# Kernel optimization log

Measured on AMD Instinct MI355X. Metric: run time of the kernel, lower is better.

Reference implementation:

```python
import jax, jax.numpy as jnp
import numpy as np

N = 100000   # nodes
R = 3        # relations
E = 500000   # edges per relation
F_IN, F_HID, F_OUT = 256, 128, 64


def setup_inputs() -> dict:
    key = jax.random.key(0)
    ks = jax.random.split(key, 9)
    feature = jax.random.normal(ks[0], (N, F_IN), jnp.float32)
    src = jax.random.randint(ks[1], (R, E), 0, N)
    dst = jax.random.randint(ks[2], (R, E), 0, N)
    neg_src = jax.random.randint(ks[3], (E,), 0, N)
    neg_dst = jax.random.randint(ks[4], (E,), 0, N)
    W1 = jax.random.normal(ks[5], (R, F_IN, F_HID), jnp.float32) * 0.05
    b1 = jnp.zeros((R, F_HID), jnp.float32)
    W2 = jax.random.normal(ks[6], (R, F_HID, F_OUT), jnp.float32) * 0.05
    b2 = jnp.zeros((R, F_OUT), jnp.float32)
    return {"feature": feature, "W1": W1, "b1": b1, "W2": W2, "b2": b2,
            "src": src, "dst": dst, "neg_src": neg_src, "neg_dst": neg_dst}


def _graph_conv(h, src, dst, W, b):
    """DGL GraphConv with norm='both': D_dst^-1/2 A (D_src^-1/2 h W) + b."""
    ones = jnp.ones(src.shape[0], h.dtype)
    out_deg = jnp.clip(jax.ops.segment_sum(ones, src, num_segments=N), 1.0)
    in_deg = jnp.clip(jax.ops.segment_sum(ones, dst, num_segments=N), 1.0)
    # project before gather (in_feats >= out_feats, same trick as DGL)
    x = (h * (out_deg ** -0.5)[:, None]) @ W          # [N, Fout]
    agg = jax.ops.segment_sum(x[src], dst, num_segments=N)  # gather-scatter
    return agg * (in_deg ** -0.5)[:, None] + b


def _hetero_layer(h, src, dst, W, b):
    # HeteroGraphConv: per-relation conv, mean-aggregate across relations
    conv = jax.vmap(_graph_conv, in_axes=(None, 0, 0, 0, 0))
    return conv(h, src, dst, W, b).mean(axis=0)


def reference(feature, W1, b1, W2, b2, src, dst, neg_src, neg_dst):
    h = jax.nn.relu(_hetero_layer(feature, src, dst, W1, b1))
    h = _hetero_layer(h, src, dst, W2, b2)             # [N, F_OUT]
    # HeteroDotProductPredictor: u_dot_v on etype (relation 0) / neg graph
    pos_score = jnp.sum(h[src[0]] * h[dst[0]], axis=-1)
    neg_score = jnp.sum(h[neg_src] * h[neg_dst], axis=-1)
    return jnp.stack([pos_score, neg_score])           # [2, E]
```

## Files before the change

### kernel.cpp

```cpp
#include <hip/hip_runtime.h>

namespace {
constexpr int NN   = 100000;
constexpr int RR   = 3;
constexpr int EE   = 500000;
constexpr int FIN  = 256;
constexpr int FHID = 128;
constexpr int FOUT = 64;
constexpr int EEC  = RR * EE;
constexpr int SCAN_TILE = 4096;
constexpr int NB = (NN + SCAN_TILE - 1) / SCAN_TILE;
constexpr int NCHUNK  = 8;
constexpr int CH      = NN / NCHUNK;
constexpr int GH      = 50;
constexpr int SLICE   = EE / GH;
constexpr int NCHUNK_F = 16;
constexpr int CH_F     = NN / NCHUNK_F;
}

typedef float f32x4  __attribute__((ext_vector_type(4)));
typedef short bf16x8 __attribute__((ext_vector_type(8)));

__device__ inline unsigned bf16round(float a) {
    unsigned u = __float_as_uint(a);
    return (u + 0x7FFFu + ((u >> 16) & 1u)) >> 16;
}
__device__ inline unsigned pack2_bf16(float a, float b) {
    return bf16round(a) | (bf16round(b) << 16);
}
__device__ inline float bflo(unsigned u) { return __uint_as_float(u << 16); }
__device__ inline float bfhi(unsigned u) { return __uint_as_float(u & 0xFFFF0000u); }

__device__ inline void gload_lds16(const unsigned short* g, unsigned short* l) {
    __builtin_amdgcn_global_load_lds(
        (const __attribute__((address_space(1))) void*)g,
        (__attribute__((address_space(3))) void*)l, 16, 0, 0);
}

__global__ __launch_bounds__(256) void convw_kernel(
    const float* __restrict__ W1, unsigned short* __restrict__ Wt1,
    const float* __restrict__ W2, unsigned short* __restrict__ Wt2)
{
    int idx = blockIdx.x * 256 + threadIdx.x;
    const int n1 = RR * FIN * FHID;
    const int n2 = RR * FHID * FOUT;
    if (idx < n1) {
        int r = idx / (FIN * FHID);
        int rem = idx - r * FIN * FHID;
        int k = rem / FHID, m = rem - k * FHID;
        Wt1[((size_t)r * FHID + m) * FIN + k] = (unsigned short)bf16round(W1[idx]);
    } else if (idx - n1 < n2) {
        int j = idx - n1;
        int r = j / (FHID * FOUT);
        int rem = j - r * FHID * FOUT;
        int k = rem / FOUT, m = rem - k * FOUT;
        Wt2[((size_t)r * FOUT + m) * FHID + k] = (unsigned short)bf16round(W2[j]);
    }
}

__global__ __launch_bounds__(512) void hist_deg_kernel(
    const int* __restrict__ src, const int* __restrict__ dst,
    unsigned short* __restrict__ partial_in, unsigned short* __restrict__ partial_out)
{
    __shared__ int cnt[CH];
    const int b   = blockIdx.x;
    const int dir = b / (RR * NCHUNK * GH);
    const int rem = b % (RR * NCHUNK * GH);
    const int r   = rem / (NCHUNK * GH);
    const int c   = (rem / GH) % NCHUNK;
    const int g   = rem % GH;
    const int tid = threadIdx.x;

    for (int i = tid; i < CH; i += 512) cnt[i] = 0;
    __syncthreads();

    const int* ids = (dir ? src : dst) + (size_t)r * EE + (size_t)g * SLICE;
    const int base = c * CH;
    for (int i4 = tid; i4 < SLICE / 4; i4 += 512) {
        int4 q = reinterpret_cast<const int4*>(ids)[i4];
        int d;
        d = q.x - base; if ((unsigned)d < (unsigned)CH) atomicAdd(&cnt[d], 1);
        d = q.y - base; if ((unsigned)d < (unsigned)CH) atomicAdd(&cnt[d], 1);
        d = q.z - base; if ((unsigned)d < (unsigned)CH) atomicAdd(&cnt[d], 1);
        d = q.w - base; if ((unsigned)d < (unsigned)CH) atomicAdd(&cnt[d], 1);
    }
    __syncthreads();

    unsigned short* part = (dir ? partial_out : partial_in)
                           + (size_t)g * RR * NN + (size_t)r * NN + base;
    for (int i = tid; i < CH; i += 512) part[i] = (unsigned short)cnt[i];
}

__global__ __launch_bounds__(256) void reduce_deg_kernel(
    const unsigned short* __restrict__ partial_in,
    const unsigned short* __restrict__ partial_out,
    int* __restrict__ deg_in, float* __restrict__ s_in, float* __restrict__ s_out)
{
    int idx = blockIdx.x * 256 + threadIdx.x;
    if (idx >= 2 * RR * NN) return;
    int dir = idx / (RR * NN);
    int j   = idx % (RR * NN);
    const unsigned short* part = dir ? partial_out : partial_in;
    int s = 0;
    #pragma unroll
    for (int g = 0; g < GH; ++g) s += part[(size_t)g * RR * NN + j];
    float v = rsqrtf((float)max(s, 1));
    if (dir == 0) { deg_in[j] = s; s_in[j] = v; }
    else          { s_out[j] = v; }
}

__global__ __launch_bounds__(1024) void scan_reduce_kernel(
    const int* __restrict__ deg_in, int* __restrict__ bsum)
{
    const int b = blockIdx.x;
    const int t = threadIdx.x;
    int n0 = b * SCAN_TILE + t * 4;
    int s = 0;
    if (n0 + 3 < NN) {
        int4 a = *reinterpret_cast<const int4*>(&deg_in[n0]);
        int4 bq = *reinterpret_cast<const int4*>(&deg_in[NN + n0]);
        int4 cq = *reinterpret_cast<const int4*>(&deg_in[2 * NN + n0]);
        s = a.x + a.y + a.z + a.w + bq.x + bq.y + bq.z + bq.w + cq.x + cq.y + cq.z + cq.w;
    } else {
        for (int i = 0; i < 4; ++i)
            if (n0 + i < NN)
                s += deg_in[n0 + i] + deg_in[NN + n0 + i] + deg_in[2 * NN + n0 + i];
    }
    __shared__ int sh[1024];
    sh[t] = s;
    __syncthreads();
    for (int off = 512; off > 0; off >>= 1) {
        if (t < off) sh[t] += sh[t + off];
        __syncthreads();
    }
    if (t == 0) bsum[b] = sh[0];
}

__global__ void scan_spine_kernel(int* __restrict__ bsum)
{
    if (threadIdx.x != 0 || blockIdx.x != 0) return;
    int run = 0;
    for (int i = 0; i < NB; ++i) {
        int v = bsum[i];
        bsum[i] = run;
        run += v;
    }
}

__global__ __launch_bounds__(1024) void scan_final_kernel(
    const int* __restrict__ deg_in, const int* __restrict__ bsum,
    int* __restrict__ rp_c)
{
    const int b = blockIdx.x;
    const int t = threadIdx.x;
    int n0 = b * SCAN_TILE + t * 4;
    int v[4] = {0, 0, 0, 0};
    for (int i = 0; i < 4; ++i)
        if (n0 + i < NN)
            v[i] = deg_in[n0 + i] + deg_in[NN + n0 + i] + deg_in[2 * NN + n0 + i];
    int s = v[0] + v[1] + v[2] + v[3];
    __shared__ int sh[1024];
    sh[t] = s;
    __syncthreads();
    for (int off = 1; off < 1024; off <<= 1) {
        int x = (t >= off) ? sh[t - off] : 0;
        __syncthreads();
        if (t >= off) sh[t] += x;
        __syncthreads();
    }
    int off = bsum[b] + sh[t] - s;
    for (int i = 0; i < 4; ++i) {
        if (n0 + i < NN) { rp_c[n0 + i] = off; off += v[i]; }
    }
    if (b == NB - 1 && t == 0) rp_c[NN] = EEC;
}

__global__ __launch_bounds__(256) void slice_off_kernel(
    const int* __restrict__ rp_c, const unsigned short* __restrict__ partial_in,
    int* __restrict__ base_c)
{
    int n = blockIdx.x * 256 + threadIdx.x;
    if (n >= NN) return;
    int base = rp_c[n];
    #pragma unroll
    for (int g = 0; g < GH; ++g) {
        base_c[(size_t)g * NN + n] = base;
        const unsigned short* p = partial_in + (size_t)g * RR * NN + n;
        base += (int)p[0] + (int)p[NN] + (int)p[2 * NN];
    }
}

__global__ __launch_bounds__(1024) void fill3_kernel(
    const int* __restrict__ src, const int* __restrict__ dst,
    const int* __restrict__ base_c, const float* __restrict__ s_in,
    uint2* __restrict__ col2)
{
    __shared__ int cur[CH_F];
    const int b   = blockIdx.x;
    const int c   = b / GH;
    const int g   = b % GH;
    const int tid = threadIdx.x;
    const int base = c * CH_F;

    const int* so = base_c + (size_t)g * NN + base;
    for (int i = tid; i < CH_F; i += 1024) cur[i] = so[i];
    __syncthreads();

    for (int r = 0; r < RR; ++r) {
        const int* ds = dst + (size_t)r * EE + (size_t)g * SLICE;
        const int* ss = src + (size_t)r * EE + (size_t)g * SLICE;
        const float* si = s_in + (size_t)r * NN;
        const unsigned rbase = (unsigned)(r * NN);
        for (int i4 = tid; i4 < SLICE / 4; i4 += 1024) {
            int4 d4 = reinterpret_cast<const int4*>(ds)[i4];
            int4 s4 = reinterpret_cast<const int4*>(ss)[i4];
            int dl;
            dl = d4.x - base;
            if ((unsigned)dl < (unsigned)CH_F) {
                int pos = atomicAdd(&cur[dl], 1);
                col2[pos] = make_uint2(rbase + (unsigned)s4.x, __float_as_uint(si[d4.x]));
            }
            dl = d4.y - base;
            if ((unsigned)dl < (unsigned)CH_F) {
                int pos = atomicAdd(&cur[dl], 1);
                col2[pos] = make_uint2(rbase + (unsigned)s4.y, __float_as_uint(si[d4.y]));
            }
            dl = d4.z - base;
            if ((unsigned)dl < (unsigned)CH_F) {
                int pos = atomicAdd(&cur[dl], 1);
                col2[pos] = make_uint2(rbase + (unsigned)s4.z, __float_as_uint(si[d4.z]));
            }
            dl = d4.w - base;
            if ((unsigned)dl < (unsigned)CH_F) {
                int pos = atomicAdd(&cur[dl], 1);
                col2[pos] = make_uint2(rbase + (unsigned)s4.w, __float_as_uint(si[d4.w]));
            }
        }
    }
}

template<int K, int CN, bool A_F32>
__global__ __launch_bounds__(256) void gemm_v6_kernel(
    const void* __restrict__ Av, const unsigned short* __restrict__ Wt_base,
    const float* __restrict__ srow_base, unsigned short* __restrict__ C_base, int N)
{
    constexpr int BM  = 64;
    constexpr int BK  = 64;
    constexpr int MF  = 2;
    constexpr int NF  = 2;
    constexpr int LDA = A_F32 ? (BK + 8) : BK;

    __shared__ unsigned short As[BM * LDA];
    __shared__ unsigned short Bs[RR][64 * BK];
    __shared__ float sLds[RR][BM];

    const int tid  = threadIdx.x;
    const int wave = tid >> 6;
    const int lane = tid & 63;
    const int wr   = wave >> 1;
    const int wc   = wave & 1;
    const int row0 = blockIdx.x * BM;
    const int bh   = blockIdx.y;
    const int l15  = lane & 15;
    const int lq   = lane >> 4;

    for (int i = tid; i < RR * BM; i += 256) {
        int r  = i / BM;
        int rr = row0 + (i % BM);
        sLds[r][i % BM] = (rr < N) ? srow_base[(size_t)r * NN + rr] : 0.f;
    }

    f32x4 acc[RR][MF][NF];
    #pragma unroll
    for (int r = 0; r < RR; ++r)
        #pragma unroll
        for (int mi = 0; mi < MF; ++mi)
            #pragma unroll
            for (int ni = 0; ni < NF; ++ni)
                #pragma unroll
                for (int q = 0; q < 4; ++q) acc[r][mi][ni][q] = 0.0f;

    for (int k0 = 0; k0 < K; k0 += BK) {
        __syncthreads();
        if constexpr (A_F32) {
            const float* A = (const float*)Av;
            #pragma unroll
            for (int i = 0; i < 2; ++i) {
                int c2  = i * 256 + tid;
                int row = c2 >> 3;
                int fc  = (c2 & 7) * 2;
                float4 v0 = make_float4(0.f, 0.f, 0.f, 0.f);
                float4 v1 = make_float4(0.f, 0.f, 0.f, 0.f);
                if (row0 + row < N) {
                    const float* Ar = A + (size_t)(row0 + row) * K + k0 + fc * 4;
                    v0 = *reinterpret_cast<const float4*>(Ar);
                    v1 = *reinterpret_cast<const float4*>(Ar + 4);
                }
                uint4 o;
                o.x = pack2_bf16(v0.x, v0.y);
                o.y = pack2_bf16(v0.z, v0.w);
                o.z = pack2_bf16(v1.x, v1.y);
                o.w = pack2_bf16(v1.z, v1.w);
                *reinterpret_cast<uint4*>(&As[row * LDA + fc * 4]) = o;
            }
        } else {
            const unsigned short* A = (const unsigned short*)Av;
            #pragma unroll
            for (int i = 0; i < 2; ++i) {
                int c   = i * 256 + tid;
                int row = c >> 3;
                int kc  = c & 7;
                int kcs = kc ^ (row & 7);
                if (row0 + row < N)
                    gload_lds16(A + (size_t)(row0 + row) * K + k0 + kcs * 8, &As[c * 8]);
            }
        }
        #pragma unroll
        for (int i = 0; i < 6; ++i) {
            int c  = i * 256 + tid;
            int r  = c >> 9;
            int cc = c & 511;
            int n  = cc >> 3;
            int kc = cc & 7;
            int kcs = kc ^ (n & 7);
            gload_lds16(Wt_base + ((size_t)r * CN + bh * 64 + n) * K + k0 + kcs * 8,
                        &Bs[r][cc * 8]);
        }
        __syncthreads();

        #pragma unroll
        for (int kk = 0; kk < BK; kk += 32) {
            const int j = kk / 8 + lq;
            bf16x8 af[MF];
            #pragma unroll
            for (int mi = 0; mi < MF; ++mi) {
                int row = wr * 32 + mi * 16 + l15;
                if constexpr (A_F32)
                    af[mi] = *reinterpret_cast<const bf16x8*>(&As[row * LDA + kk + lq * 8]);
                else
                    af[mi] = *reinterpret_cast<const bf16x8*>(&As[row * BK + (j ^ (row & 7)) * 8]);
            }
            #pragma unroll
            for (int r = 0; r < RR; ++r) {
                bf16x8 bfg[NF];
                #pragma unroll
                for (int ni = 0; ni < NF; ++ni) {
                    int n = wc * 32 + ni * 16 + l15;
                    bfg[ni] = *reinterpret_cast<const bf16x8*>(&Bs[r][n * BK + (j ^ (n & 7)) * 8]);
                }
                #pragma unroll
                for (int mi = 0; mi < MF; ++mi)
                    #pragma unroll
                    for (int ni = 0; ni < NF; ++ni)
                        acc[r][mi][ni] = __builtin_amdgcn_mfma_f32_16x16x32_bf16(
                            af[mi], bfg[ni], acc[r][mi][ni], 0, 0, 0);
            }
        }
    }

    #pragma unroll
    for (int r = 0; r < RR; ++r) {
        unsigned short* C = C_base + (size_t)r * NN * CN;
        #pragma unroll
        for (int mi = 0; mi < MF; ++mi) {
            int lrow = wr * 32 + mi * 16 + lq * 4;
            #pragma unroll
            for (int ni = 0; ni < NF; ++ni) {
                int cc = bh * 64 + wc * 32 + ni * 16 + l15;
                #pragma unroll
                for (int q = 0; q < 4; ++q) {
                    int rr = row0 + lrow + q;
                    if (rr < N)
                        C[(size_t)rr * CN + cc] =
                            (unsigned short)bf16round(acc[r][mi][ni][q] * sLds[r][lrow + q]);
                }
            }
        }
    }
}

__global__ __launch_bounds__(256) void gather1_kernel(
    const unsigned* __restrict__ Y, const uint2* __restrict__ col2,
    const int* __restrict__ rp_c, const float* __restrict__ b1,
    unsigned* __restrict__ h1)
{
    const int wid  = threadIdx.x >> 6;
    const int lane = threadIdx.x & 63;
    const int n    = blockIdx.x * 4 + wid;
    if (n >= NN) return;
    const int beg = rp_c[n], end = rp_c[n + 1];

    float ax[8], ay[8];
    #pragma unroll
    for (int j = 0; j < 8; ++j) { ax[j] = 0.f; ay[j] = 0.f; }

    int e = beg;
    for (; e + 7 < end; e += 8) {
        uint2 cc[8]; unsigned uu[8];
        #pragma unroll
        for (int j = 0; j < 8; ++j) cc[j] = col2[e + j];
        #pragma unroll
        for (int j = 0; j < 8; ++j) uu[j] = Y[(size_t)cc[j].x * 64 + lane];
        #pragma unroll
        for (int j = 0; j < 8; ++j) {
            float s = __uint_as_float(cc[j].y);
            ax[j] = fmaf(s, bflo(uu[j]), ax[j]);
            ay[j] = fmaf(s, bfhi(uu[j]), ay[j]);
        }
    }
    for (; e + 3 < end; e += 4) {
        uint2 cc[4]; unsigned uu[4];
        #pragma unroll
        for (int j = 0; j < 4; ++j) cc[j] = col2[e + j];
        #pragma unroll
        for (int j = 0; j < 4; ++j) uu[j] = Y[(size_t)cc[j].x * 64 + lane];
        #pragma unroll
        for (int j = 0; j < 4; ++j) {
            float s = __uint_as_float(cc[j].y);
            ax[j] = fmaf(s, bflo(uu[j]), ax[j]);
            ay[j] = fmaf(s, bfhi(uu[j]), ay[j]);
        }
    }
    for (; e < end; ++e) {
        uint2 c0 = col2[e];
        unsigned u0 = Y[(size_t)c0.x * 64 + lane];
        float s = __uint_as_float(c0.y);
        ax[0] = fmaf(s, bflo(u0), ax[0]);
        ay[0] = fmaf(s, bfhi(u0), ay[0]);
    }
    float sx = ((ax[0] + ax[1]) + (ax[2] + ax[3])) + ((ax[4] + ax[5]) + (ax[6] + ax[7]));
    float sy = ((ay[0] + ay[1]) + (ay[2] + ay[3])) + ((ay[4] + ay[5]) + (ay[6] + ay[7]));
    float bx = b1[lane * 2]     + b1[FHID + lane * 2]     + b1[2 * FHID + lane * 2];
    float by = b1[lane * 2 + 1] + b1[FHID + lane * 2 + 1] + b1[2 * FHID + lane * 2 + 1];
    const float inv = 1.0f / (float)RR;
    float ox = fmaxf((sx + bx) * inv, 0.f);
    float oy = fmaxf((sy + by) * inv, 0.f);
    h1[(size_t)n * 64 + lane] = pack2_bf16(ox, oy);
}

__global__ __launch_bounds__(256) void gather2_kernel(
    const unsigned short* __restrict__ Y, const uint2* __restrict__ col2,
    const int* __restrict__ rp_c, const float* __restrict__ b2,
    unsigned short* __restrict__ h2)
{
    const int wid  = threadIdx.x >> 6;
    const int lane = threadIdx.x & 63;
    const int n    = blockIdx.x * 4 + wid;
    if (n >= NN) return;
    const int beg = rp_c[n], end = rp_c[n + 1];

    float a[8];
    #pragma unroll
    for (int j = 0; j < 8; ++j) a[j] = 0.f;

    int e = beg;
    for (; e + 7 < end; e += 8) {
        uint2 cc[8]; unsigned short uu[8];
        #pragma unroll
        for (int j = 0; j < 8; ++j) cc[j] = col2[e + j];
        #pragma unroll
        for (int j = 0; j < 8; ++j) uu[j] = Y[(size_t)cc[j].x * 64 + lane];
        #pragma unroll
        for (int j = 0; j < 8; ++j)
            a[j] = fmaf(__uint_as_float(cc[j].y),
                        __uint_as_float((unsigned)uu[j] << 16), a[j]);
    }
    for (; e + 3 < end; e += 4) {
        uint2 cc[4]; unsigned short uu[4];
        #pragma unroll
        for (int j = 0; j < 4; ++j) cc[j] = col2[e + j];
        #pragma unroll
        for (int j = 0; j < 4; ++j) uu[j] = Y[(size_t)cc[j].x * 64 + lane];
        #pragma unroll
        for (int j = 0; j < 4; ++j)
            a[j] = fmaf(__uint_as_float(cc[j].y),
                        __uint_as_float((unsigned)uu[j] << 16), a[j]);
    }
    for (; e < end; ++e) {
        uint2 c0 = col2[e];
        a[0] = fmaf(__uint_as_float(c0.y),
                    __uint_as_float((unsigned)Y[(size_t)c0.x * 64 + lane] << 16), a[0]);
    }
    float s = ((a[0] + a[1]) + (a[2] + a[3])) + ((a[4] + a[5]) + (a[6] + a[7]));
    float bs = b2[lane] + b2[FOUT + lane] + b2[2 * FOUT + lane];
    float o = (s + bs) * (1.0f / (float)RR);
    h2[(size_t)n * 64 + lane] = (unsigned short)bf16round(o);
}

__global__ __launch_bounds__(256) void score_kernel(
    const unsigned short* __restrict__ h, const int* __restrict__ src0,
    const int* __restrict__ dst0, const int* __restrict__ nsrc,
    const int* __restrict__ ndst, float* __restrict__ out)
{
    int idx = blockIdx.x * 256 + threadIdx.x;
    int e = idx >> 3;
    int l = idx & 7;
    int u, v;
    if (e < EE) { u = src0[e]; v = dst0[e]; }
    else        { u = nsrc[e - EE]; v = ndst[e - EE]; }
    uint4 a = *reinterpret_cast<const uint4*>(&h[(size_t)u * FOUT + l * 8]);
    uint4 b = *reinterpret_cast<const uint4*>(&h[(size_t)v * FOUT + l * 8]);
    float p = bflo(a.x) * bflo(b.x) + bfhi(a.x) * bfhi(b.x)
            + bflo(a.y) * bflo(b.y) + bfhi(a.y) * bfhi(b.y)
            + bflo(a.z) * bflo(b.z) + bfhi(a.z) * bfhi(b.z)
            + bflo(a.w) * bflo(b.w) + bfhi(a.w) * bfhi(b.w);
    p += __shfl_xor(p, 4, 8);
    p += __shfl_xor(p, 2, 8);
    p += __shfl_xor(p, 1, 8);
    if (l == 0) out[e] = p;
}

extern "C" void kernel_launch(void* const* d_in, const int* in_sizes, int n_in,
                              void* d_out, int out_size, void* d_ws, size_t ws_size,
                              hipStream_t stream)
{
    const float* feature = (const float*)d_in[0];
    const float* W1      = (const float*)d_in[1];
    const float* b1      = (const float*)d_in[2];
    const float* W2      = (const float*)d_in[3];
    const float* b2      = (const float*)d_in[4];
    const int*   src     = (const int*)d_in[5];
    const int*   dst     = (const int*)d_in[6];
    const int*   nsrc    = (const int*)d_in[7];
    const int*   ndst    = (const int*)d_in[8];
    float* out = (float*)d_out;

    char* p = (char*)d_ws;
    float* s_out   = (float*)p; p += sizeof(float) * RR * NN;
    float* s_in    = (float*)p; p += sizeof(float) * RR * NN;
    unsigned* h1   = (unsigned*)p; p += sizeof(unsigned) * (size_t)NN * 64;
    unsigned short* h2 = (unsigned short*)p; p += sizeof(unsigned short) * (size_t)NN * FOUT;
    char*  Yu      = p;         p += (size_t)RR * NN * FHID * 2;
    int*   deg_in  = (int*)p;   p += sizeof(int) * RR * NN;
    int*   rp_c    = (int*)p;   p += sizeof(int) * (NN + 1);
    uint2* col2    = (uint2*)p; p += sizeof(uint2) * (size_t)EEC;
    int*   bsum    = (int*)p;   p += sizeof(int) * NB;
    unsigned short* Wt1 = (unsigned short*)p; p += sizeof(unsigned short) * RR * FIN * FHID;
    unsigned short* Wt2 = (unsigned short*)p; p += sizeof(unsigned short) * RR * FHID * FOUT;

    unsigned short* Y1 = (unsigned short*)Yu;
    unsigned short* Y2 = (unsigned short*)Yu;
    unsigned short* partial_in  = (unsigned short*)Yu;
    unsigned short* partial_out = partial_in + (size_t)GH * RR * NN;
    int* base_c = (int*)partial_out;

    convw_kernel<<<(RR * FIN * FHID + RR * FHID * FOUT + 255) / 256, 256, 0, stream>>>(
        W1, Wt1, W2, Wt2);
    hist_deg_kernel<<<2 * RR * NCHUNK * GH, 512, 0, stream>>>(
        src, dst, partial_in, partial_out);
    reduce_deg_kernel<<<(2 * RR * NN + 255) / 256, 256, 0, stream>>>(
        partial_in, partial_out, deg_in, s_in, s_out);
    scan_reduce_kernel<<<NB, 1024, 0, stream>>>(deg_in, bsum);
    scan_spine_kernel<<<1, 64, 0, stream>>>(bsum);
    scan_final_kernel<<<NB, 1024, 0, stream>>>(deg_in, bsum, rp_c);
    slice_off_kernel<<<(NN + 255) / 256, 256, 0, stream>>>(rp_c, partial_in, base_c);
    fill3_kernel<<<NCHUNK_F * GH, 1024, 0, stream>>>(src, dst, base_c, s_in, col2);

    const int node_grid = (NN + 3) / 4;

    gemm_v6_kernel<FIN, FHID, true><<<dim3((NN + 63) / 64, 2), 256, 0, stream>>>(
        feature, Wt1, s_out, Y1, NN);
    gather1_kernel<<<node_grid, 256, 0, stream>>>(
        (const unsigned*)Y1, col2, rp_c, b1, h1);

    gemm_v6_kernel<FHID, FOUT, false><<<dim3((NN + 63) / 64, 1), 256, 0, stream>>>(
        h1, Wt2, s_out, Y2, NN);
    gather2_kernel<<<node_grid, 256, 0, stream>>>(
        Y2, col2, rp_c, b2, h2);

    score_kernel<<<(2 * EE * 8) / 256, 256, 0, stream>>>(h2, src, dst, nsrc, ndst, out);
}
```

Baseline: 341.6 us.

## Merge CSR fill kernel and layer-1 GEMM into one launch with block-range dispatch

Combines the edge fill into the CSR column array and the first-layer projection GEMM into a single kernel. The first FILL_BLOCKS block ids do the fill and the remaining ids do GEMM tiles, so the latency-bound, atomic-heavy fill can overlap with the MFMA GEMM instead of running serially. Fill blocks shrink from 1024 to 256 threads to match the GEMM block size, which means more loop iterations per block. Y1 shares memory with base_c, so GEMM writes can race with fill blocks still reading base_c if scheduling does not put the fill reads first.

```diff
diff --git a/kernel.cpp b/kernel.cpp
--- a/kernel.cpp
+++ b/kernel.cpp
@@ -16,6 +16,7 @@
 constexpr int SLICE   = EE / GH;
 constexpr int NCHUNK_F = 16;
 constexpr int CH_F     = NN / NCHUNK_F;
+constexpr int FILL_BLOCKS = NCHUNK_F * GH;
 }
 
 typedef float f32x4  __attribute__((ext_vector_type(4)));
@@ -190,50 +191,196 @@
     }
 }
 
-__global__ __launch_bounds__(1024) void fill3_kernel(
+template<int K, int CN, bool A_F32>
+__global__ __launch_bounds__(256) void mega_fill_gemm_kernel(
     const int* __restrict__ src, const int* __restrict__ dst,
     const int* __restrict__ base_c, const float* __restrict__ s_in,
-    uint2* __restrict__ col2)
-{
-    __shared__ int cur[CH_F];
-    const int b   = blockIdx.x;
-    const int c   = b / GH;
-    const int g   = b % GH;
+    uint2* __restrict__ col2,
+    const void* __restrict__ Av, const unsigned short* __restrict__ Wt_base,
+    const float* __restrict__ srow_base, unsigned short* __restrict__ C_base,
+    int N, int gemm_gx)
+{
+    constexpr int BM  = 64;
+    constexpr int BK  = 64;
+    constexpr int MF  = 2;
+    constexpr int NF  = 2;
+    constexpr int LDA = A_F32 ? (BK + 8) : BK;
+
+    __shared__ __align__(16) char smem[(size_t)BM * LDA * 2 + RR * 64 * BK * 2 + RR * BM * 4];
+
     const int tid = threadIdx.x;
-    const int base = c * CH_F;
-
-    const int* so = base_c + (size_t)g * NN + base;
-    for (int i = tid; i < CH_F; i += 1024) cur[i] = so[i];
-    __syncthreads();
-
+
+    if ((int)blockIdx.x < FILL_BLOCKS) {
+        int* cur = (int*)smem;
+        const int b    = blockIdx.x;
+        const int c    = b / GH;
+        const int g    = b % GH;
+        const int base = c * CH_F;
+
+        const int* so = base_c + (size_t)g * NN + base;
+        for (int i = tid; i < CH_F; i += 256) cur[i] = so[i];
+        __syncthreads();
+
+        for (int r = 0; r < RR; ++r) {
+            const int* ds = dst + (size_t)r * EE + (size_t)g * SLICE;
+            const int* ss = src + (size_t)r * EE + (size_t)g * SLICE;
+            const float* si = s_in + (size_t)r * NN;
+            const unsigned rbase = (unsigned)(r * NN);
+            for (int i4 = tid; i4 < SLICE / 4; i4 += 256) {
+                int4 d4 = reinterpret_cast<const int4*>(ds)[i4];
+                int4 s4 = reinterpret_cast<const int4*>(ss)[i4];
+                int dl;
+                dl = d4.x - base;
+                if ((unsigned)dl < (unsigned)CH_F) {
+                    int pos = atomicAdd(&cur[dl], 1);
+                    col2[pos] = make_uint2(rbase + (unsigned)s4.x, __float_as_uint(si[d4.x]));
+                }
+                dl = d4.y - base;
+                if ((unsigned)dl < (unsigned)CH_F) {
+                    int pos = atomicAdd(&cur[dl], 1);
+                    col2[pos] = make_uint2(rbase + (unsigned)s4.y, __float_as_uint(si[d4.y]));
+                }
+                dl = d4.z - base;
+                if ((unsigned)dl < (unsigned)CH_F) {
+                    int pos = atomicAdd(&cur[dl], 1);
+                    col2[pos] = make_uint2(rbase + (unsigned)s4.z, __float_as_uint(si[d4.z]));
+                }
+                dl = d4.w - base;
+                if ((unsigned)dl < (unsigned)CH_F) {
+                    int pos = atomicAdd(&cur[dl], 1);
+                    col2[pos] = make_uint2(rbase + (unsigned)s4.w, __float_as_uint(si[d4.w]));
+                }
+            }
+        }
+        return;
+    }
+
+    unsigned short* As  = (unsigned short*)smem;
+    unsigned short* Bs  = As + (size_t)BM * LDA;
+    float*          sLds = (float*)(Bs + (size_t)RR * 64 * BK);
+
+    const int gid  = (int)blockIdx.x - FILL_BLOCKS;
+    const int bx   = gid % gemm_gx;
+    const int bh   = gid / gemm_gx;
+    const int wave = tid >> 6;
+    const int lane = tid & 63;
+    const int wr   = wave >> 1;
+    const int wc   = wave & 1;
+    const int row0 = bx * BM;
+    const int l15  = lane & 15;
+    const int lq   = lane >> 4;
+
+    for (int i = tid; i < RR * BM; i += 256) {
+        int r  = i / BM;
+        int rr = row0 + (i % BM);
+        sLds[i] = (rr < N) ? srow_base[(size_t)r * NN + rr] : 0.f;
+    }
+
+    f32x4 acc[RR][MF][NF];
+    #pragma unroll
+    for (int r = 0; r < RR; ++r)
+        #pragma unroll
+        for (int mi = 0; mi < MF; ++mi)
+            #pragma unroll
+            for (int ni = 0; ni < NF; ++ni)
+                #pragma unroll
+                for (int q = 0; q < 4; ++q) acc[r][mi][ni][q] = 0.0f;
+
+    for (int k0 = 0; k0 < K; k0 += BK) {
+        __syncthreads();
+        if constexpr (A_F32) {
+            const float* A = (const float*)Av;
+            #pragma unroll
+            for (int i = 0; i < 2; ++i) {
+                int c2  = i * 256 + tid;
+                int row = c2 >> 3;
+                int fc  = (c2 & 7) * 2;
+                float4 v0 = make_float4(0.f, 0.f, 0.f, 0.f);
+                float4 v1 = make_float4(0.f, 0.f, 0.f, 0.f);
+                if (row0 + row < N) {
+                    const float* Ar = A + (size_t)(row0 + row) * K + k0 + fc * 4;
+                    v0 = *reinterpret_cast<const float4*>(Ar);
+                    v1 = *reinterpret_cast<const float4*>(Ar + 4);
+                }
+                uint4 o;
+                o.x = pack2_bf16(v0.x, v0.y);
+                o.y = pack2_bf16(v0.z, v0.w);
+                o.z = pack2_bf16(v1.x, v1.y);
+                o.w = pack2_bf16(v1.z, v1.w);
+                *reinterpret_cast<uint4*>(&As[row * LDA + fc * 4]) = o;
+            }
+        } else {
+            const unsigned short* A = (const unsigned short*)Av;
+            #pragma unroll
+            for (int i = 0; i < 2; ++i) {
+                int c   = i * 256 + tid;
+                int row = c >> 3;
+                int kc  = c & 7;
+                int kcs = kc ^ (row & 7);
+                if (row0 + row < N)
+                    gload_lds16(A + (size_t)(row0 + row) * K + k0 + kcs * 8, &As[c * 8]);
+            }
+        }
+        #pragma unroll
+        for (int i = 0; i < 6; ++i) {
+            int c  = i * 256 + tid;
+            int r  = c >> 9;
+            int cc = c & 511;
+            int n  = cc >> 3;
+            int kc = cc & 7;
+            int kcs = kc ^ (n & 7);
+            gload_lds16(Wt_base + ((size_t)r * CN + bh * 64 + n) * K + k0 + kcs * 8,
+                        &Bs[(size_t)r * 64 * BK + cc * 8]);
+        }
+        __syncthreads();
+
+        #pragma unroll
+        for (int kk = 0; kk < BK; kk += 32) {
+            const int j = kk / 8 + lq;
+            bf16x8 af[MF];
+            #pragma unroll
+            for (int mi = 0; mi < MF; ++mi) {
+                int row = wr * 32 + mi * 16 + l15;
+                if constexpr (A_F32)
+                    af[mi] = *reinterpret_cast<const bf16x8*>(&As[row * LDA + kk + lq * 8]);
+                else
+                    af[mi] = *reinterpret_cast<const bf16x8*>(&As[row * BK + (j ^ (row & 7)) * 8]);
+            }
+            #pragma unroll
+            for (int r = 0; r < RR; ++r) {
+                bf16x8 bfg[NF];
+                #pragma unroll
+                for (int ni = 0; ni < NF; ++ni) {
+                    int n = wc * 32 + ni * 16 + l15;
+                    bfg[ni] = *reinterpret_cast<const bf16x8*>(
+                        &Bs[(size_t)r * 64 * BK + n * BK + (j ^ (n & 7)) * 8]);
+                }
+                #pragma unroll
+                for (int mi = 0; mi < MF; ++mi)
+                    #pragma unroll
+                    for (int ni = 0; ni < NF; ++ni)
+                        acc[r][mi][ni] = __builtin_amdgcn_mfma_f32_16x16x32_bf16(
+                            af[mi], bfg[ni], acc[r][mi][ni], 0, 0, 0);
+            }
+        }
+    }
+
+    #pragma unroll
     for (int r = 0; r < RR; ++r) {
-        const int* ds = dst + (size_t)r * EE + (size_t)g * SLICE;
-        const int* ss = src + (size_t)r * EE + (size_t)g * SLICE;
-        const float* si = s_in + (size_t)r * NN;
-        const unsigned rbase = (unsigned)(r * NN);
-        for (int i4 = tid; i4 < SLICE / 4; i4 += 1024) {
-            int4 d4 = reinterpret_cast<const int4*>(ds)[i4];
-            int4 s4 = reinterpret_cast<const int4*>(ss)[i4];
-            int dl;
-            dl = d4.x - base;
-            if ((unsigned)dl < (unsigned)CH_F) {
-                int pos = atomicAdd(&cur[dl], 1);
-                col2[pos] = make_uint2(rbase + (unsigned)s4.x, __float_as_uint(si[d4.x]));
-            }
-            dl = d4.y - base;
-            if ((unsigned)dl < (unsigned)CH_F) {
-                int pos = atomicAdd(&cur[dl], 1);
-                col2[pos] = make_uint2(rbase + (unsigned)s4.y, __float_as_uint(si[d4.y]));
-            }
-            dl = d4.z - base;
-            if ((unsigned)dl < (unsigned)CH_F) {
-                int pos = atomicAdd(&cur[dl], 1);
-                col2[pos] = make_uint2(rbase + (unsigned)s4.z, __float_as_uint(si[d4.z]));
-            }
-            dl = d4.w - base;
-            if ((unsigned)dl < (unsigned)CH_F) {
-                int pos = atomicAdd(&cur[dl], 1);
-                col2[pos] = make_uint2(rbase + (unsigned)s4.w, __float_as_uint(si[d4.w]));
+        unsigned short* C = C_base + (size_t)r * NN * CN;
+        #pragma unroll
+        for (int mi = 0; mi < MF; ++mi) {
+            int lrow = wr * 32 + mi * 16 + lq * 4;
+            #pragma unroll
+            for (int ni = 0; ni < NF; ++ni) {
+                int cc = bh * 64 + wc * 32 + ni * 16 + l15;
+                #pragma unroll
+                for (int q = 0; q < 4; ++q) {
+                    int rr = row0 + lrow + q;
+                    if (rr < N)
+                        C[(size_t)rr * CN + cc] =
+                            (unsigned short)bf16round(acc[r][mi][ni][q] * sLds[r * BM + lrow + q]);
+                }
             }
         }
     }
@@ -554,16 +701,18 @@
     scan_spine_kernel<<<1, 64, 0, stream>>>(bsum);
     scan_final_kernel<<<NB, 1024, 0, stream>>>(deg_in, bsum, rp_c);
     slice_off_kernel<<<(NN + 255) / 256, 256, 0, stream>>>(rp_c, partial_in, base_c);
-    fill3_kernel<<<NCHUNK_F * GH, 1024, 0, stream>>>(src, dst, base_c, s_in, col2);
 
     const int node_grid = (NN + 3) / 4;
-
-    gemm_v6_kernel<FIN, FHID, true><<<dim3((NN + 63) / 64, 2), 256, 0, stream>>>(
-        feature, Wt1, s_out, Y1, NN);
+    const int gemm_gx = (NN + 63) / 64;
+
+    mega_fill_gemm_kernel<FIN, FHID, true><<<FILL_BLOCKS + gemm_gx * 2, 256, 0, stream>>>(
+        src, dst, base_c, s_in, col2,
+        feature, Wt1, s_out, Y1, NN, gemm_gx);
+
     gather1_kernel<<<node_grid, 256, 0, stream>>>(
         (const unsigned*)Y1, col2, rp_c, b1, h1);
 
-    gemm_v6_kernel<FHID, FOUT, false><<<dim3((NN + 63) / 64, 1), 256, 0, stream>>>(
+    gemm_v6_kernel<FHID, FOUT, false><<<dim3(gemm_gx, 1), 256, 0, stream>>>(
         h1, Wt2, s_out, Y2, NN);
     gather2_kernel<<<node_grid, 256, 0, stream>>>(
         Y2, col2, rp_c, b2, h2);
```

Result: no change. 343.5 us (+0.6%).
